# Optimization experiments

Measured on AMD Instinct MI355X. Metric: run time of the kernel, lower is better.

## Reference

```python
import jax, jax.numpy as jnp
import numpy as np

D = 3  # hardcoded window half-width in the module


def setup_inputs() -> dict:
    key = jax.random.key(0)
    ks = jax.random.split(key, 5)
    B, T, S = 16, 1024, 4096
    q_size, c_size, p_size = 512, 512, 512
    q = jax.random.normal(ks[0], (B, q_size, S), jnp.float32)
    c_t = jax.random.normal(ks[1], (B, T, c_size), jnp.float32)
    # torch nn.Linear weight layouts: (out_features, in_features)
    W_a = jax.random.normal(ks[2], (c_size, q_size), jnp.float32) / np.sqrt(q_size).astype(np.float32)
    W_p = jax.random.normal(ks[3], (p_size, c_size), jnp.float32) / np.sqrt(c_size).astype(np.float32)
    V_p = jax.random.normal(ks[4], (1, p_size), jnp.float32) / np.sqrt(p_size).astype(np.float32)
    return {"q": q, "c_t": c_t, "W_a": W_a, "W_p": W_p, "V_p": V_p}


def reference(q, c_t, W_a, W_p, V_p):
    B, q_size, S = q.shape
    # predictive alignment: p_t = S * sigmoid(V_p tanh(W_p c_t)) -> (B, T, 1)
    p_t = S * jax.nn.sigmoid(jnp.tanh(c_t @ W_p.T) @ V_p.T)
    # pad one NaN column at the front of the sequence, then (B, S+1, q_size)
    q_pad = jnp.pad(q, ((0, 0), (0, 0), (1, 0)), constant_values=jnp.nan).transpose(0, 2, 1)
    # window indices: clamp(long(p_t) + idx + 1, 0, S+1) % (S+1), idx in [-D, D]
    offsets = jnp.arange(-D + 1, D + 2)  # (2D+1,)
    s = jnp.clip(p_t.astype(jnp.int32) + offsets[None, None, :], 0, S + 1) % (S + 1)  # (B,T,2D+1)
    # per-batch gather of the local window: (B, T, 2D+1, q_size)
    qg = q_pad[jnp.arange(B)[:, None, None], s]
    nan_loc = jnp.isnan(qg[..., 0])  # (B, T, 2D+1)
    qg = jnp.where(nan_loc[..., None], 0.0, qg)
    # score: dot(W_a q, c_t) -> (B, T, 2D+1)
    a_t = jnp.einsum('btwq,cq,btc->btw', qg, W_a, c_t)
    a_t = jnp.where(nan_loc, -jnp.inf, a_t)
    attn = jax.nn.softmax(a_t, axis=2)
    # Gaussian decay around predicted position p_t
    gauss = jnp.exp(-2.0 * ((jnp.clip(s.astype(jnp.float32) - 1.0, 0.0, None) - p_t) / D) ** 2)
    W_attn = attn * gauss
    out = jnp.einsum('btw,btwq->btq', W_attn, qg)  # (B, T, q_size)
    return out
```

## Files before the change

kernel.cpp:

```cpp
#include <hip/hip_runtime.h>
#include <hip/hip_bf16.h>

#define BB 16
#define TT 1024
#define SS 4096
#define CS 512
#define QS 512
#define PS 512
#define NROW (BB*TT)

typedef unsigned short ushort_t;
typedef unsigned int u32;
typedef short bf16x8 __attribute__((ext_vector_type(8)));
typedef float f32x4 __attribute__((ext_vector_type(4)));

#define AS1 __attribute__((address_space(1)))
#define AS3 __attribute__((address_space(3)))

__device__ __forceinline__ void gl2l16(const void* g, void* l) {
    __builtin_amdgcn_global_load_lds((const AS1 u32*)g, (AS3 u32*)l, 16, 0, 0);
}

__device__ __forceinline__ ushort_t f2bf(float f) {
    u32 x = __float_as_uint(f);
    return (ushort_t)((x + 0x7fffu + ((x >> 16) & 1u)) >> 16);
}
__device__ __forceinline__ float bf2f(ushort_t b) {
    return __uint_as_float(((u32)b) << 16);
}

__global__ __launch_bounds__(256) void k_conv_a(const float* __restrict__ c,
                                                ushort_t* __restrict__ A) {
    const int i = blockIdx.x * 256 + threadIdx.x;
    const int m = i >> 7;
    const int k = (i & 127) * 4;
    float4 v = *(const float4*)(c + (size_t)m * CS + k);
    ushort4 hi, lo;
    hi.x = f2bf(v.x); lo.x = f2bf(v.x - bf2f(hi.x));
    hi.y = f2bf(v.y); lo.y = f2bf(v.y - bf2f(hi.y));
    hi.z = f2bf(v.z); lo.z = f2bf(v.z - bf2f(hi.z));
    hi.w = f2bf(v.w); lo.w = f2bf(v.w - bf2f(hi.w));
    *(ushort4*)(A + (size_t)m * 1024 + k)       = hi;
    *(ushort4*)(A + (size_t)m * 1024 + 512 + k) = lo;
}

__global__ __launch_bounds__(256) void k_conv_b(const float* __restrict__ Wa,
                                                const float* __restrict__ Wp,
                                                ushort_t* __restrict__ B,
                                                int* __restrict__ cnt) {
    const int n = blockIdx.x;
    const int t = threadIdx.x;
    if (n == 0 && t < 2) cnt[t] = 0;
    #pragma unroll
    for (int kk = 0; kk < 2; ++kk) {
        const int k = t + 256 * kk;
        float v = (n < 512) ? Wa[(size_t)k * QS + n] : Wp[(size_t)(n - 512) * CS + k];
        ushort_t hi = f2bf(v);
        ushort_t lo = f2bf(v - bf2f(hi));
        B[(size_t)n * 1024 + k]       = hi;
        B[(size_t)n * 1024 + 512 + k] = lo;
    }
}

__global__ __launch_bounds__(256) void k_tq(const float* __restrict__ q,
                                            float* __restrict__ qT) {
    __shared__ float t[64][65];
    const int b  = blockIdx.z;
    const int s0 = blockIdx.x * 64;
    const int d0 = blockIdx.y * 64;
    const int tx = threadIdx.x & 15;
    const int ty = threadIdx.x >> 4;
    const float* qb = q + ((size_t)b * QS + d0) * SS + s0;
    #pragma unroll
    for (int i = 0; i < 4; ++i) {
        float4 v = *(const float4*)(qb + (size_t)(ty + 16 * i) * SS + tx * 4);
        *(float4*)&t[ty + 16 * i][tx * 4] = v;
    }
    __syncthreads();
    float* qo = qT + ((size_t)b * SS + s0) * QS + d0;
    #pragma unroll
    for (int i = 0; i < 4; ++i) {
        const int s = ty + 16 * i;
        float4 v = make_float4(t[tx * 4 + 0][s], t[tx * 4 + 1][s],
                               t[tx * 4 + 2][s], t[tx * 4 + 3][s]);
        *(float4*)(qo + (size_t)s * QS + tx * 4) = v;
    }
}

__global__ __launch_bounds__(512, 2) void k_gemm(const ushort_t* __restrict__ A,
                                                 const ushort_t* __restrict__ B,
                                                 const float* __restrict__ V_p,
                                                 float* __restrict__ u,
                                                 float* __restrict__ zpart) {
    __shared__ ushort_t lds[8][8192];
    const int tid = threadIdx.x;
    const int l = tid & 63;
    const int w = tid >> 6;
    const int wm = w >> 2;
    const int wn = w & 3;
    const int ln = l & 15, lh = l >> 4;

    const int orig = blockIdx.x;
    const int swz = ((orig & 7) << 5) + (orig >> 3);
    const int m0 = (swz >> 2) * 256;
    const int nt = swz & 3;
    const int n0 = nt * 256;

    const int srow = tid >> 2;
    const int scg  = tid & 3;
    const int scol0 = (scg ^ ((srow >> 1) & 3)) * 8;

    const int swzr = (lh ^ ((ln >> 1) & 3)) << 3;
    int aoffL[2][4], boffL[4];
    #pragma unroll
    for (int ms = 0; ms < 2; ++ms)
        #pragma unroll
        for (int mi = 0; mi < 4; ++mi)
            aoffL[ms][mi] = (wm * 128 + ms * 64 + mi * 16 + ln) * 32 + swzr;
    #pragma unroll
    for (int ni = 0; ni < 4; ++ni)
        boffL[ni] = (wn * 64 + ni * 16 + ln) * 32 + swzr;

    f32x4 acc[8][4];
    #pragma unroll
    for (int a = 0; a < 8; ++a)
        #pragma unroll
        for (int b2 = 0; b2 < 4; ++b2) acc[a][b2] = (f32x4){0.f, 0.f, 0.f, 0.f};

    auto STAGE = [&](int c) {
        const int tt = c >> 2, rem = c & 3, kh = rem >> 1;
        const int blk = tt >> 3, k0 = (tt & 7) << 6;
        const ushort_t* src;
        if (rem & 1) {
            const int boff = (blk == 1) ? 512 : 0;
            src = B + (size_t)(n0 + srow) * 1024 + boff + k0 + kh * 32 + scol0;
        } else {
            const int aoff = (blk == 2) ? 512 : 0;
            src = A + (size_t)(m0 + srow) * 1024 + aoff + k0 + kh * 32 + scol0;
        }
        ushort_t* dst = &lds[c & 7][tid * 8];
        gl2l16(src, dst);
        gl2l16(src + 128 * 1024, dst + 4096);
    };

    #pragma unroll
    for (int c = 0; c < 6; ++c) STAGE(c);
    asm volatile("s_waitcnt vmcnt(4)" ::: "memory");
    __builtin_amdgcn_s_barrier();

    #pragma unroll 1
    for (int t = 0; t < 24; ++t) {
        #pragma unroll
        for (int P = 0; P < 2; ++P) {
            const int sA = ((t << 2) + (P << 1)) & 7;
            const int sB = sA + 1;
            const ushort_t* bA = &lds[sA][0];
            const ushort_t* bB = &lds[sB][0];
            bf16x8 af[8], bb[4];
            #pragma unroll
            for (int mi = 0; mi < 4; ++mi) {
                af[mi]     = *(const bf16x8*)(bA + aoffL[0][mi]);
                af[4 + mi] = *(const bf16x8*)(bA + aoffL[1][mi]);
            }
            #pragma unroll
            for (int ni = 0; ni < 4; ++ni)
                bb[ni] = *(const bf16x8*)(bB + boffL[ni]);
            const int c0 = (t << 2) + (P << 1) + 6;
            if (c0 <= 95) STAGE(c0);
            if (c0 + 1 <= 95) STAGE(c0 + 1);
            __builtin_amdgcn_s_setprio(1);
            #pragma unroll
            for (int ms = 0; ms < 2; ++ms)
                #pragma unroll
                for (int mi = 0; mi < 4; ++mi)
                    #pragma unroll
                    for (int ni = 0; ni < 4; ++ni)
                        acc[ms * 4 + mi][ni] = __builtin_amdgcn_mfma_f32_16x16x32_bf16(
                            af[ms * 4 + mi], bb[ni], acc[ms * 4 + mi][ni], 0, 0, 0);
            __builtin_amdgcn_s_setprio(0);
            if (P == 1) {
                if (t == 22) { asm volatile("s_waitcnt vmcnt(0)" ::: "memory"); }
                else if (t < 22) { asm volatile("s_waitcnt vmcnt(4)" ::: "memory"); }
            }
            __builtin_amdgcn_s_barrier();
        }
    }

    if (nt < 2) {
        #pragma unroll
        for (int mg = 0; mg < 8; ++mg) {
            #pragma unroll
            for (int r = 0; r < 4; ++r) {
                const int m = m0 + wm * 128 + mg * 16 + lh * 4 + r;
                float* up = u + (size_t)m * QS + nt * 256 + wn * 64 + ln;
                #pragma unroll
                for (int ni = 0; ni < 4; ++ni) up[ni * 16] = acc[mg][ni][r];
            }
        }
    } else {
        float vp[4];
        #pragma unroll
        for (int ni = 0; ni < 4; ++ni)
            vp[ni] = V_p[(nt - 2) * 256 + wn * 64 + ni * 16 + ln];
        #pragma unroll
        for (int mg = 0; mg < 8; ++mg) {
            #pragma unroll
            for (int r = 0; r < 4; ++r) {
                float sv = 0.f;
                #pragma unroll
                for (int ni = 0; ni < 4; ++ni) sv += tanhf(acc[mg][ni][r]) * vp[ni];
                sv += __shfl_xor(sv, 1, 64);
                sv += __shfl_xor(sv, 2, 64);
                sv += __shfl_xor(sv, 4, 64);
                sv += __shfl_xor(sv, 8, 64);
                if (ln == 0)
                    zpart[(size_t)(m0 + wm * 128 + mg * 16 + lh * 4 + r) * 8 +
                          (nt - 2) * 4 + wn] = sv;
            }
        }
    }
}

__global__ __launch_bounds__(256) void k_z(const float* __restrict__ zpart,
                                           float* __restrict__ pt, int* __restrict__ tr,
                                           int* __restrict__ list1, int* __restrict__ cnt1) {
    const int row = blockIdx.x * 256 + threadIdx.x;
    const float4 a = *(const float4*)(zpart + (size_t)row * 8);
    const float4 b = *(const float4*)(zpart + (size_t)row * 8 + 4);
    float z = ((a.x + a.y) + (a.z + a.w)) + ((b.x + b.y) + (b.z + b.w));
    float ptv = 4096.f / (1.f + expf(-z));
    float fr = ptv - floorf(ptv);
    pt[row] = ptv;
    tr[row] = (int)ptv;
    if (fr < 0.06f || fr > 0.94f) {
        int i = atomicAdd(cnt1, 1);
        list1[i] = row;
    }
}

__global__ __launch_bounds__(256) void k_rep1(
    const float* __restrict__ c_t, const float* __restrict__ W_p,
    const float* __restrict__ V_p, float* __restrict__ pt, int* __restrict__ tr,
    const int* __restrict__ list1, const int* __restrict__ cnt1,
    int* __restrict__ list2, int* __restrict__ cnt2)
{
    const int tid = threadIdx.x;
    const int lane = tid & 63;
    const int wid = tid >> 6;
    const int n1 = cnt1[0];
    __shared__ float cl[8][132 * 4];
    __shared__ double zl[4][8];
    __shared__ int rows_s[8];

    for (int g0 = blockIdx.x * 8; g0 < n1; g0 += gridDim.x * 8) {
        const int nr = min(8, n1 - g0);
        __syncthreads();
        if (tid < nr) rows_s[tid] = list1[g0 + tid];
        __syncthreads();
        for (int idx = tid; idx < nr * 128; idx += 256) {
            int r = idx >> 7, k = (idx & 127) * 4;
            *(float4*)&cl[r][k] = *(const float4*)(c_t + (size_t)rows_s[r] * CS + k);
        }
        __syncthreads();

        const float* wp0 = W_p + (size_t)tid * CS;
        const float* wp1 = W_p + (size_t)(tid + 256) * CS;
        f32x4 acc[2][8];
        #pragma unroll
        for (int p = 0; p < 2; ++p)
            #pragma unroll
            for (int r = 0; r < 8; ++r) acc[p][r] = (f32x4){0.f, 0.f, 0.f, 0.f};

        for (int k = 0; k < CS; k += 16) {
            f32x4 w0[4], w1[4];
            #pragma unroll
            for (int j = 0; j < 4; ++j) {
                w0[j] = *(const f32x4*)(wp0 + k + 4 * j);
                w1[j] = *(const f32x4*)(wp1 + k + 4 * j);
            }
            #pragma unroll
            for (int j = 0; j < 4; ++j) {
                #pragma unroll
                for (int r = 0; r < 8; ++r) {
                    f32x4 c4 = *(const f32x4*)&cl[r][k + 4 * j];
                    acc[0][r] += c4 * w0[j];
                    acc[1][r] += c4 * w1[j];
                }
            }
        }

        const float vp0 = V_p[tid];
        const float vp1 = V_p[tid + 256];
        double zp[8];
        #pragma unroll
        for (int r = 0; r < 8; ++r) {
            float X0 = (acc[0][r][0] + acc[0][r][1]) + (acc[0][r][2] + acc[0][r][3]);
            float X1 = (acc[1][r][0] + acc[1][r][1]) + (acc[1][r][2] + acc[1][r][3]);
            zp[r] = (double)(tanhf(X0) * vp0) + (double)(tanhf(X1) * vp1);
        }
        #pragma unroll
        for (int r = 0; r < 8; ++r) {
            double v = zp[r];
            #pragma unroll
            for (int o = 32; o > 0; o >>= 1) v += __shfl_down(v, o, 64);
            if (lane == 0) zl[wid][r] = v;
        }
        __syncthreads();
        if (tid < nr) {
            double z = (zl[0][tid] + zl[1][tid]) + (zl[2][tid] + zl[3][tid]);
            double ptv = 4096.0 / (1.0 + exp(-z));
            const int row = rows_s[tid];
            pt[row] = (float)ptv;
            tr[row] = (int)ptv;
            double fr = ptv - floor(ptv);
            if (fr < 5e-3 || fr > 0.995) {
                int i2 = atomicAdd(cnt2, 1);
                list2[i2] = row;
            }
        }
    }
}

__global__ __launch_bounds__(256) void k_rep2a(
    const float* __restrict__ c_t, const float* __restrict__ W_p,
    const float* __restrict__ V_p,
    const int* __restrict__ list2, const int* __restrict__ cnt2,
    double* __restrict__ zp2)
{
    const int tid = threadIdx.x;
    const int pl = tid & 63;
    const int kq = tid >> 6;
    const int n2 = cnt2[0];
    __shared__ float cl[CS];
    __shared__ double xsh[4][64];

    for (int i = blockIdx.x; i < n2 * 8; i += gridDim.x) {
        const int li = i >> 3;
        const int pc = i & 7;
        const int row = list2[li];
        const int p0 = pc * 64;
        __syncthreads();
        if (tid < 128)
            *(float4*)(cl + tid * 4) = *(const float4*)(c_t + (size_t)row * CS + tid * 4);
        __syncthreads();
        const float* wr = W_p + (size_t)(p0 + pl) * CS + kq * 128;
        const float* cr = cl + kq * 128;
        double Xa = 0.0, Xb = 0.0, Xc = 0.0, Xd = 0.0;
        #pragma unroll 4
        for (int k = 0; k < 128; k += 4) {
            float4 w4 = *(const float4*)(wr + k);
            float4 c4 = *(const float4*)(cr + k);
            Xa += (double)c4.x * w4.x;
            Xb += (double)c4.y * w4.y;
            Xc += (double)c4.z * w4.z;
            Xd += (double)c4.w * w4.w;
        }
        xsh[kq][pl] = (Xa + Xb) + (Xc + Xd);
        __syncthreads();
        if (tid < 64) {
            double X = (xsh[0][pl] + xsh[1][pl]) + (xsh[2][pl] + xsh[3][pl]);
            double zv = tanh(X) * (double)V_p[p0 + pl];
            #pragma unroll
            for (int o = 32; o > 0; o >>= 1) zv += __shfl_down(zv, o, 64);
            if (pl == 0) zp2[i] = zv;
        }
    }
}

__global__ __launch_bounds__(256) void k_rep2b(
    const double* __restrict__ zp2, const int* __restrict__ list2,
    const int* __restrict__ cnt2, float* __restrict__ pt, int* __restrict__ tr)
{
    const int idx = blockIdx.x * 256 + threadIdx.x;
    if (idx >= cnt2[0]) return;
    const double* zr = zp2 + (size_t)idx * 8;
    double z = 0.0;
    #pragma unroll
    for (int j = 0; j < 8; ++j) z += zr[j];
    double ptv = 4096.0 / (1.0 + exp(-z));
    const int row = list2[idx];
    pt[row] = (float)ptv;
    tr[row] = (int)ptv;
}

__global__ __launch_bounds__(256) void k_attn_t(
    const float* __restrict__ qT, const float* __restrict__ u,
    const float* __restrict__ pt, const int* __restrict__ tr,
    float* __restrict__ out)
{
    const int wid = threadIdx.x >> 6;
    const int lane = threadIdx.x & 63;
    const int bt = blockIdx.x * 4 + wid;
    const int b = bt >> 10;

    const float* urow = u + (size_t)bt * QS;
    float4 ua = *(const float4*)(urow + lane * 8);
    float4 ub = *(const float4*)(urow + lane * 8 + 4);
    float uv[8] = {ua.x, ua.y, ua.z, ua.w, ub.x, ub.y, ub.z, ub.w};

    const float ptv = pt[bt];
    const int tn = tr[bt];
    const float* qTb = qT + (size_t)b * SS * QS;

    bool val[7];
    int pos[7];
    #pragma unroll
    for (int w = 0; w < 7; ++w) {
        int sv = tn + w - 2;
        sv = sv < 0 ? 0 : (sv > SS + 1 ? SS + 1 : sv);
        if (sv == SS + 1) sv = 0;
        val[w] = (sv != 0);
        pos[w] = sv - 1;
    }

    float qg[7][8];
    #pragma unroll
    for (int w = 0; w < 7; ++w) {
        if (val[w]) {
            const float* qr = qTb + (size_t)pos[w] * QS + lane * 8;
            float4 a = *(const float4*)qr;
            float4 c = *(const float4*)(qr + 4);
            qg[w][0] = a.x; qg[w][1] = a.y; qg[w][2] = a.z; qg[w][3] = a.w;
            qg[w][4] = c.x; qg[w][5] = c.y; qg[w][6] = c.z; qg[w][7] = c.w;
        } else {
            #pragma unroll
            for (int j = 0; j < 8; ++j) qg[w][j] = 0.f;
        }
    }

    float at[7];
    #pragma unroll
    for (int w = 0; w < 7; ++w) {
        float p = 0.f;
        #pragma unroll
        for (int j = 0; j < 8; ++j) p = fmaf(qg[w][j], uv[j], p);
        #pragma unroll
        for (int o = 1; o < 64; o <<= 1) p += __shfl_xor(p, o, 64);
        at[w] = p;
    }

    float m = -1e30f;
    #pragma unroll
    for (int w = 0; w < 7; ++w) if (val[w]) m = fmaxf(m, at[w]);
    float e[7], den = 0.f;
    #pragma unroll
    for (int w = 0; w < 7; ++w) { e[w] = val[w] ? expf(at[w] - m) : 0.f; den += e[w]; }
    const float inv = 1.f / den;

    float acc[8] = {0.f, 0.f, 0.f, 0.f, 0.f, 0.f, 0.f, 0.f};
    #pragma unroll
    for (int w = 0; w < 7; ++w) {
        if (val[w]) {
            float d = ((float)pos[w] - ptv) * (1.f / 3.f);
            float wt = e[w] * inv * expf(-2.f * d * d);
            #pragma unroll
            for (int j = 0; j < 8; ++j) acc[j] = fmaf(wt, qg[w][j], acc[j]);
        }
    }

    float* orow = out + (size_t)bt * QS + lane * 8;
    *(float4*)orow       = make_float4(acc[0], acc[1], acc[2], acc[3]);
    *(float4*)(orow + 4) = make_float4(acc[4], acc[5], acc[6], acc[7]);
}

__global__ __launch_bounds__(256) void k_attn_g(
    const float* __restrict__ q, const float* __restrict__ u,
    const float* __restrict__ pt, const int* __restrict__ tr,
    float* __restrict__ out)
{
    const int wid = threadIdx.x >> 6;
    const int lane = threadIdx.x & 63;
    const int bt = blockIdx.x * 4 + wid;
    const int b = bt >> 10;

    const float* urow = u + (size_t)bt * QS;
    float4 ua = *(const float4*)(urow + lane * 8);
    float4 ub = *(const float4*)(urow + lane * 8 + 4);
    float uv[8] = {ua.x, ua.y, ua.z, ua.w, ub.x, ub.y, ub.z, ub.w};

    const float ptv = pt[bt];
    const int tn = tr[bt];
    const float* qb = q + (size_t)b * QS * SS;

    bool val[7];
    int pos[7];
    #pragma unroll
    for (int w = 0; w < 7; ++w) {
        int sv = tn + w - 2;
        sv = sv < 0 ? 0 : (sv > SS + 1 ? SS + 1 : sv);
        if (sv == SS + 1) sv = 0;
        val[w] = (sv != 0);
        pos[w] = sv - 1;
    }

    float qg[7][8];
    #pragma unroll
    for (int j = 0; j < 8; ++j) {
        const float* qrow = qb + (size_t)(lane * 8 + j) * SS;
        #pragma unroll
        for (int w = 0; w < 7; ++w)
            qg[w][j] = val[w] ? qrow[pos[w]] : 0.f;
    }

    float at[7];
    #pragma unroll
    for (int w = 0; w < 7; ++w) {
        float p = 0.f;
        #pragma unroll
        for (int j = 0; j < 8; ++j) p = fmaf(qg[w][j], uv[j], p);
        #pragma unroll
        for (int o = 1; o < 64; o <<= 1) p += __shfl_xor(p, o, 64);
        at[w] = p;
    }

    float m = -1e30f;
    #pragma unroll
    for (int w = 0; w < 7; ++w) if (val[w]) m = fmaxf(m, at[w]);
    float e[7], den = 0.f;
    #pragma unroll
    for (int w = 0; w < 7; ++w) { e[w] = val[w] ? expf(at[w] - m) : 0.f; den += e[w]; }
    const float inv = 1.f / den;

    float acc[8] = {0.f, 0.f, 0.f, 0.f, 0.f, 0.f, 0.f, 0.f};
    #pragma unroll
    for (int w = 0; w < 7; ++w) {
        if (val[w]) {
            float d = ((float)pos[w] - ptv) * (1.f / 3.f);
            float wt = e[w] * inv * expf(-2.f * d * d);
            #pragma unroll
            for (int j = 0; j < 8; ++j) acc[j] = fmaf(wt, qg[w][j], acc[j]);
        }
    }

    float* orow = out + (size_t)bt * QS + lane * 8;
    *(float4*)orow       = make_float4(acc[0], acc[1], acc[2], acc[3]);
    *(float4*)(orow + 4) = make_float4(acc[4], acc[5], acc[6], acc[7]);
}

extern "C" void kernel_launch(void* const* d_in, const int* in_sizes, int n_in,
                              void* d_out, int out_size, void* d_ws, size_t ws_size,
                              hipStream_t stream) {
    const float* q   = (const float*)d_in[0];
    const float* c_t = (const float*)d_in[1];
    const float* W_a = (const float*)d_in[2];
    const float* W_p = (const float*)d_in[3];
    const float* V_p = (const float*)d_in[4];
    float* out = (float*)d_out;

    char* ws = (char*)d_ws;
    ushort_t* Ap  = (ushort_t*)(ws);
    ushort_t* Bp  = (ushort_t*)(ws + 33554432);
    float*    u   = (float*)  (ws + 35651584);
    float*    zp  = (float*)  (ws + 69206016);
    float*    pt  = (float*)  (ws + 69730304);
    int*      tr  = (int*)    (ws + 69795840);
    int*      l1  = (int*)    (ws + 69861376);
    int*      l2  = (int*)    (ws + 69926912);
    int*      cnt = (int*)    (ws + 69992448);
    double*   zp2 = (double*) (ws + 70000640);
    float*    qT  = (float*)  (ws + 73400320);
    const bool use_T = (ws_size >= 73400320ULL + 134217728ULL);

    hipLaunchKernelGGL(k_conv_a, dim3(8192), dim3(256), 0, stream, c_t, Ap);
    hipLaunchKernelGGL(k_conv_b, dim3(1024), dim3(256), 0, stream, W_a, W_p, Bp, cnt);
    if (use_T)
        hipLaunchKernelGGL(k_tq, dim3(64, 8, 16), dim3(256), 0, stream, q, qT);
    hipLaunchKernelGGL(k_gemm, dim3(256), dim3(512), 0, stream, Ap, Bp, V_p, u, zp);
    hipLaunchKernelGGL(k_z, dim3(64), dim3(256), 0, stream, zp, pt, tr, l1, cnt);
    hipLaunchKernelGGL(k_rep1, dim3(512), dim3(256), 0, stream,
                       c_t, W_p, V_p, pt, tr, l1, cnt, l2, cnt + 1);
    hipLaunchKernelGGL(k_rep2a, dim3(512), dim3(256), 0, stream,
                       c_t, W_p, V_p, l2, cnt + 1, zp2);
    hipLaunchKernelGGL(k_rep2b, dim3(64), dim3(256), 0, stream,
                       zp2, l2, cnt + 1, pt, tr);
    if (use_T)
        hipLaunchKernelGGL(k_attn_t, dim3(NROW / 4), dim3(256), 0, stream, qT, u, pt, tr, out);
    else
        hipLaunchKernelGGL(k_attn_g, dim3(NROW / 4), dim3(256), 0, stream, q, u, pt, tr, out);
}
```

Baseline: 249.3 us.

## Load GEMM B fragments from global, rewrite transpose without LDS, reorder launches

The GEMM main loop now streams only the A operand through LDS with global_load_lds. B fragments are loaded straight from global memory into registers and double-buffered across half-steps, with explicit waitcnt and sched barriers placed around the MFMA blocks. This is meant to halve LDS staging traffic and raise MFMA density, at the cost of more global loads and VGPR pressure under the 512x2 launch bound. The q transpose kernel drops its LDS tile in favour of a per-thread 4x4 register transpose, and it now launches just before the attention kernel instead of before the GEMM.

```diff
diff --git a/kernel.cpp b/kernel.cpp
--- a/kernel.cpp
+++ b/kernel.cpp
@@ -64,27 +64,19 @@
 
 __global__ __launch_bounds__(256) void k_tq(const float* __restrict__ q,
                                             float* __restrict__ qT) {
-    __shared__ float t[64][65];
     const int b  = blockIdx.z;
-    const int s0 = blockIdx.x * 64;
-    const int d0 = blockIdx.y * 64;
-    const int tx = threadIdx.x & 15;
-    const int ty = threadIdx.x >> 4;
+    const int s0 = blockIdx.x * 64 + (threadIdx.x & 15) * 4;
+    const int d0 = blockIdx.y * 64 + (threadIdx.x >> 4) * 4;
     const float* qb = q + ((size_t)b * QS + d0) * SS + s0;
-    #pragma unroll
-    for (int i = 0; i < 4; ++i) {
-        float4 v = *(const float4*)(qb + (size_t)(ty + 16 * i) * SS + tx * 4);
-        *(float4*)&t[ty + 16 * i][tx * 4] = v;
-    }
-    __syncthreads();
+    float4 v0 = *(const float4*)(qb);
+    float4 v1 = *(const float4*)(qb + SS);
+    float4 v2 = *(const float4*)(qb + 2 * SS);
+    float4 v3 = *(const float4*)(qb + 3 * SS);
     float* qo = qT + ((size_t)b * SS + s0) * QS + d0;
-    #pragma unroll
-    for (int i = 0; i < 4; ++i) {
-        const int s = ty + 16 * i;
-        float4 v = make_float4(t[tx * 4 + 0][s], t[tx * 4 + 1][s],
-                               t[tx * 4 + 2][s], t[tx * 4 + 3][s]);
-        *(float4*)(qo + (size_t)s * QS + tx * 4) = v;
-    }
+    *(float4*)(qo)          = make_float4(v0.x, v1.x, v2.x, v3.x);
+    *(float4*)(qo + QS)     = make_float4(v0.y, v1.y, v2.y, v3.y);
+    *(float4*)(qo + 2 * QS) = make_float4(v0.z, v1.z, v2.z, v3.z);
+    *(float4*)(qo + 3 * QS) = make_float4(v0.w, v1.w, v2.w, v3.w);
 }
 
 __global__ __launch_bounds__(512, 2) void k_gemm(const ushort_t* __restrict__ A,
@@ -111,15 +103,14 @@
     const int scol0 = (scg ^ ((srow >> 1) & 3)) * 8;
 
     const int swzr = (lh ^ ((ln >> 1) & 3)) << 3;
-    int aoffL[2][4], boffL[4];
+    int aoffL[2][4];
     #pragma unroll
     for (int ms = 0; ms < 2; ++ms)
         #pragma unroll
         for (int mi = 0; mi < 4; ++mi)
             aoffL[ms][mi] = (wm * 128 + ms * 64 + mi * 16 + ln) * 32 + swzr;
-    #pragma unroll
-    for (int ni = 0; ni < 4; ++ni)
-        boffL[ni] = (wn * 64 + ni * 16 + ln) * 32 + swzr;
+
+    const ushort_t* bbase = B + (size_t)(n0 + wn * 64 + ln) * 1024 + lh * 8;
 
     f32x4 acc[8][4];
     #pragma unroll
@@ -127,63 +118,67 @@
         #pragma unroll
         for (int b2 = 0; b2 < 4; ++b2) acc[a][b2] = (f32x4){0.f, 0.f, 0.f, 0.f};
 
-    auto STAGE = [&](int c) {
-        const int tt = c >> 2, rem = c & 3, kh = rem >> 1;
-        const int blk = tt >> 3, k0 = (tt & 7) << 6;
-        const ushort_t* src;
-        if (rem & 1) {
-            const int boff = (blk == 1) ? 512 : 0;
-            src = B + (size_t)(n0 + srow) * 1024 + boff + k0 + kh * 32 + scol0;
-        } else {
-            const int aoff = (blk == 2) ? 512 : 0;
-            src = A + (size_t)(m0 + srow) * 1024 + aoff + k0 + kh * 32 + scol0;
-        }
+    bf16x8 af[8], bb0[4], bb1[4];
+
+    auto STAGEA = [&](int c) {
+        const int tt2 = c >> 1, kh2 = c & 1;
+        const int blk2 = tt2 >> 3, k02 = (tt2 & 7) << 6;
+        const int aoff2 = (blk2 == 2) ? 512 : 0;
+        const ushort_t* src = A + (size_t)(m0 + srow) * 1024 + aoff2 + k02 +
+                              kh2 * 32 + scol0;
         ushort_t* dst = &lds[c & 7][tid * 8];
         gl2l16(src, dst);
         gl2l16(src + 128 * 1024, dst + 4096);
     };
-
-    #pragma unroll
-    for (int c = 0; c < 6; ++c) STAGE(c);
+    auto LOADB = [&](bf16x8* bbv, int g) {
+        const int tt2 = g >> 1, kh2 = g & 1;
+        const int blk2 = tt2 >> 3;
+        const int off2 = ((blk2 == 1) ? 512 : 0) + ((tt2 & 7) << 6) + kh2 * 32;
+        #pragma unroll
+        for (int ni = 0; ni < 4; ++ni)
+            bbv[ni] = *(const bf16x8*)(bbase + (size_t)ni * 16 * 1024 + off2);
+    };
+    auto LDA = [&](int slot) {
+        const ushort_t* bA = &lds[slot][0];
+        #pragma unroll
+        for (int ms = 0; ms < 2; ++ms)
+            #pragma unroll
+            for (int mi = 0; mi < 4; ++mi)
+                af[ms * 4 + mi] = *(const bf16x8*)(bA + aoffL[ms][mi]);
+    };
+    auto MFMAC = [&](const bf16x8* bbv) {
+        asm volatile("s_waitcnt vmcnt(6)" ::: "memory");
+        asm volatile("s_waitcnt lgkmcnt(0)" ::: "memory");
+        __builtin_amdgcn_sched_barrier(0);
+        __builtin_amdgcn_s_setprio(1);
+        #pragma unroll
+        for (int ms = 0; ms < 2; ++ms)
+            #pragma unroll
+            for (int mi = 0; mi < 4; ++mi)
+                #pragma unroll
+                for (int ni = 0; ni < 4; ++ni)
+                    acc[ms * 4 + mi][ni] = __builtin_amdgcn_mfma_f32_16x16x32_bf16(
+                        af[ms * 4 + mi], bbv[ni], acc[ms * 4 + mi][ni], 0, 0, 0);
+        __builtin_amdgcn_s_setprio(0);
+        __builtin_amdgcn_s_barrier();
+    };
+
+    #pragma unroll
+    for (int c = 0; c < 6; ++c) STAGEA(c);
+    LOADB(bb0, 0);
     asm volatile("s_waitcnt vmcnt(4)" ::: "memory");
     __builtin_amdgcn_s_barrier();
 
     #pragma unroll 1
     for (int t = 0; t < 24; ++t) {
-        #pragma unroll
-        for (int P = 0; P < 2; ++P) {
-            const int sA = ((t << 2) + (P << 1)) & 7;
-            const int sB = sA + 1;
-            const ushort_t* bA = &lds[sA][0];
-            const ushort_t* bB = &lds[sB][0];
-            bf16x8 af[8], bb[4];
-            #pragma unroll
-            for (int mi = 0; mi < 4; ++mi) {
-                af[mi]     = *(const bf16x8*)(bA + aoffL[0][mi]);
-                af[4 + mi] = *(const bf16x8*)(bA + aoffL[1][mi]);
-            }
-            #pragma unroll
-            for (int ni = 0; ni < 4; ++ni)
-                bb[ni] = *(const bf16x8*)(bB + boffL[ni]);
-            const int c0 = (t << 2) + (P << 1) + 6;
-            if (c0 <= 95) STAGE(c0);
-            if (c0 + 1 <= 95) STAGE(c0 + 1);
-            __builtin_amdgcn_s_setprio(1);
-            #pragma unroll
-            for (int ms = 0; ms < 2; ++ms)
-                #pragma unroll
-                for (int mi = 0; mi < 4; ++mi)
-                    #pragma unroll
-                    for (int ni = 0; ni < 4; ++ni)
-                        acc[ms * 4 + mi][ni] = __builtin_amdgcn_mfma_f32_16x16x32_bf16(
-                            af[ms * 4 + mi], bb[ni], acc[ms * 4 + mi][ni], 0, 0, 0);
-            __builtin_amdgcn_s_setprio(0);
-            if (P == 1) {
-                if (t == 22) { asm volatile("s_waitcnt vmcnt(0)" ::: "memory"); }
-                else if (t < 22) { asm volatile("s_waitcnt vmcnt(4)" ::: "memory"); }
-            }
-            __builtin_amdgcn_s_barrier();
-        }
+        LDA((2 * t) & 7);
+        LOADB(bb1, 2 * t + 1);
+        if (2 * t + 6 <= 47) STAGEA(2 * t + 6);
+        MFMAC(bb0);
+        LDA((2 * t + 1) & 7);
+        if (t < 23) LOADB(bb0, 2 * t + 2);
+        if (2 * t + 7 <= 47) STAGEA(2 * t + 7);
+        MFMAC(bb1);
     }
 
     if (nt < 2) {
@@ -563,8 +558,6 @@
 
     hipLaunchKernelGGL(k_conv_a, dim3(8192), dim3(256), 0, stream, c_t, Ap);
     hipLaunchKernelGGL(k_conv_b, dim3(1024), dim3(256), 0, stream, W_a, W_p, Bp, cnt);
-    if (use_T)
-        hipLaunchKernelGGL(k_tq, dim3(64, 8, 16), dim3(256), 0, stream, q, qT);
     hipLaunchKernelGGL(k_gemm, dim3(256), dim3(512), 0, stream, Ap, Bp, V_p, u, zp);
     hipLaunchKernelGGL(k_z, dim3(64), dim3(256), 0, stream, zp, pt, tr, l1, cnt);
     hipLaunchKernelGGL(k_rep1, dim3(512), dim3(256), 0, stream,
@@ -573,8 +566,10 @@
                        c_t, W_p, V_p, l2, cnt + 1, zp2);
     hipLaunchKernelGGL(k_rep2b, dim3(64), dim3(256), 0, stream,
                        zp2, l2, cnt + 1, pt, tr);
-    if (use_T)
+    if (use_T) {
+        hipLaunchKernelGGL(k_tq, dim3(64, 8, 16), dim3(256), 0, stream, q, qT);
         hipLaunchKernelGGL(k_attn_t, dim3(NROW / 4), dim3(256), 0, stream, qT, u, pt, tr, out);
-    else
+    } else {
         hipLaunchKernelGGL(k_attn_g, dim3(NROW / 4), dim3(256), 0, stream, q, u, pt, tr, out);
-}
+    }
+}
```

New measurement: 270.1 us. 8.3% more time.

## Use 1024-thread GEMM blocks, register-only q transpose, and reorder transpose launch

Applied to the files above, without the earlier changes.

The GEMM block grows from 8 to 16 waves, each wave owning a 64x64 tile instead of 128x64. Each thread now stages one 16-byte chunk instead of two, and the vmcnt waits are adjusted to match. The q transpose drops its LDS tile and swaps 4x4 float4 blocks in registers, which makes each store row a strided 16-byte write. The transpose launch moves to just before the attention kernel, presumably so its output is fresher in cache when consumed. Risks are occupancy limits at 1024 threads with launch_bounds(1024,4), and poorer coalescing in the transpose stores.

```diff
diff --git a/kernel.cpp b/kernel.cpp
--- a/kernel.cpp
+++ b/kernel.cpp
@@ -64,34 +64,26 @@
 
 __global__ __launch_bounds__(256) void k_tq(const float* __restrict__ q,
                                             float* __restrict__ qT) {
-    __shared__ float t[64][65];
     const int b  = blockIdx.z;
-    const int s0 = blockIdx.x * 64;
-    const int d0 = blockIdx.y * 64;
-    const int tx = threadIdx.x & 15;
-    const int ty = threadIdx.x >> 4;
+    const int s0 = blockIdx.x * 64 + (threadIdx.x & 15) * 4;
+    const int d0 = blockIdx.y * 64 + (threadIdx.x >> 4) * 4;
     const float* qb = q + ((size_t)b * QS + d0) * SS + s0;
-    #pragma unroll
-    for (int i = 0; i < 4; ++i) {
-        float4 v = *(const float4*)(qb + (size_t)(ty + 16 * i) * SS + tx * 4);
-        *(float4*)&t[ty + 16 * i][tx * 4] = v;
-    }
-    __syncthreads();
+    float4 v0 = *(const float4*)(qb);
+    float4 v1 = *(const float4*)(qb + SS);
+    float4 v2 = *(const float4*)(qb + 2 * SS);
+    float4 v3 = *(const float4*)(qb + 3 * SS);
     float* qo = qT + ((size_t)b * SS + s0) * QS + d0;
-    #pragma unroll
-    for (int i = 0; i < 4; ++i) {
-        const int s = ty + 16 * i;
-        float4 v = make_float4(t[tx * 4 + 0][s], t[tx * 4 + 1][s],
-                               t[tx * 4 + 2][s], t[tx * 4 + 3][s]);
-        *(float4*)(qo + (size_t)s * QS + tx * 4) = v;
-    }
-}
-
-__global__ __launch_bounds__(512, 2) void k_gemm(const ushort_t* __restrict__ A,
-                                                 const ushort_t* __restrict__ B,
-                                                 const float* __restrict__ V_p,
-                                                 float* __restrict__ u,
-                                                 float* __restrict__ zpart) {
+    *(float4*)(qo)          = make_float4(v0.x, v1.x, v2.x, v3.x);
+    *(float4*)(qo + QS)     = make_float4(v0.y, v1.y, v2.y, v3.y);
+    *(float4*)(qo + 2 * QS) = make_float4(v0.z, v1.z, v2.z, v3.z);
+    *(float4*)(qo + 3 * QS) = make_float4(v0.w, v1.w, v2.w, v3.w);
+}
+
+__global__ __launch_bounds__(1024, 4) void k_gemm(const ushort_t* __restrict__ A,
+                                                  const ushort_t* __restrict__ B,
+                                                  const float* __restrict__ V_p,
+                                                  float* __restrict__ u,
+                                                  float* __restrict__ zpart) {
     __shared__ ushort_t lds[8][8192];
     const int tid = threadIdx.x;
     const int l = tid & 63;
@@ -111,19 +103,17 @@
     const int scol0 = (scg ^ ((srow >> 1) & 3)) * 8;
 
     const int swzr = (lh ^ ((ln >> 1) & 3)) << 3;
-    int aoffL[2][4], boffL[4];
-    #pragma unroll
-    for (int ms = 0; ms < 2; ++ms)
-        #pragma unroll
-        for (int mi = 0; mi < 4; ++mi)
-            aoffL[ms][mi] = (wm * 128 + ms * 64 + mi * 16 + ln) * 32 + swzr;
+    int aoffL[4], boffL[4];
+    #pragma unroll
+    for (int mi = 0; mi < 4; ++mi)
+        aoffL[mi] = (wm * 64 + mi * 16 + ln) * 32 + swzr;
     #pragma unroll
     for (int ni = 0; ni < 4; ++ni)
         boffL[ni] = (wn * 64 + ni * 16 + ln) * 32 + swzr;
 
-    f32x4 acc[8][4];
-    #pragma unroll
-    for (int a = 0; a < 8; ++a)
+    f32x4 acc[4][4];
+    #pragma unroll
+    for (int a = 0; a < 4; ++a)
         #pragma unroll
         for (int b2 = 0; b2 < 4; ++b2) acc[a][b2] = (f32x4){0.f, 0.f, 0.f, 0.f};
 
@@ -138,14 +128,12 @@
             const int aoff = (blk == 2) ? 512 : 0;
             src = A + (size_t)(m0 + srow) * 1024 + aoff + k0 + kh * 32 + scol0;
         }
-        ushort_t* dst = &lds[c & 7][tid * 8];
-        gl2l16(src, dst);
-        gl2l16(src + 128 * 1024, dst + 4096);
+        gl2l16(src, &lds[c & 7][tid * 8]);
     };
 
     #pragma unroll
     for (int c = 0; c < 6; ++c) STAGE(c);
-    asm volatile("s_waitcnt vmcnt(4)" ::: "memory");
+    asm volatile("s_waitcnt vmcnt(2)" ::: "memory");
     __builtin_amdgcn_s_barrier();
 
     #pragma unroll 1
@@ -156,12 +144,10 @@
             const int sB = sA + 1;
             const ushort_t* bA = &lds[sA][0];
             const ushort_t* bB = &lds[sB][0];
-            bf16x8 af[8], bb[4];
-            #pragma unroll
-            for (int mi = 0; mi < 4; ++mi) {
-                af[mi]     = *(const bf16x8*)(bA + aoffL[0][mi]);
-                af[4 + mi] = *(const bf16x8*)(bA + aoffL[1][mi]);
-            }
+            bf16x8 af[4], bb[4];
+            #pragma unroll
+            for (int mi = 0; mi < 4; ++mi)
+                af[mi] = *(const bf16x8*)(bA + aoffL[mi]);
             #pragma unroll
             for (int ni = 0; ni < 4; ++ni)
                 bb[ni] = *(const bf16x8*)(bB + boffL[ni]);
@@ -170,17 +156,15 @@
             if (c0 + 1 <= 95) STAGE(c0 + 1);
             __builtin_amdgcn_s_setprio(1);
             #pragma unroll
-            for (int ms = 0; ms < 2; ++ms)
+            for (int mi = 0; mi < 4; ++mi)
                 #pragma unroll
-                for (int mi = 0; mi < 4; ++mi)
-                    #pragma unroll
-                    for (int ni = 0; ni < 4; ++ni)
-                        acc[ms * 4 + mi][ni] = __builtin_amdgcn_mfma_f32_16x16x32_bf16(
-                            af[ms * 4 + mi], bb[ni], acc[ms * 4 + mi][ni], 0, 0, 0);
+                for (int ni = 0; ni < 4; ++ni)
+                    acc[mi][ni] = __builtin_amdgcn_mfma_f32_16x16x32_bf16(
+                        af[mi], bb[ni], acc[mi][ni], 0, 0, 0);
             __builtin_amdgcn_s_setprio(0);
             if (P == 1) {
                 if (t == 22) { asm volatile("s_waitcnt vmcnt(0)" ::: "memory"); }
-                else if (t < 22) { asm volatile("s_waitcnt vmcnt(4)" ::: "memory"); }
+                else if (t < 22) { asm volatile("s_waitcnt vmcnt(2)" ::: "memory"); }
             }
             __builtin_amdgcn_s_barrier();
         }
@@ -188,13 +172,13 @@
 
     if (nt < 2) {
         #pragma unroll
-        for (int mg = 0; mg < 8; ++mg) {
+        for (int mi = 0; mi < 4; ++mi) {
             #pragma unroll
             for (int r = 0; r < 4; ++r) {
-                const int m = m0 + wm * 128 + mg * 16 + lh * 4 + r;
+                const int m = m0 + wm * 64 + mi * 16 + lh * 4 + r;
                 float* up = u + (size_t)m * QS + nt * 256 + wn * 64 + ln;
                 #pragma unroll
-                for (int ni = 0; ni < 4; ++ni) up[ni * 16] = acc[mg][ni][r];
+                for (int ni = 0; ni < 4; ++ni) up[ni * 16] = acc[mi][ni][r];
             }
         }
     } else {
@@ -203,18 +187,18 @@
         for (int ni = 0; ni < 4; ++ni)
             vp[ni] = V_p[(nt - 2) * 256 + wn * 64 + ni * 16 + ln];
         #pragma unroll
-        for (int mg = 0; mg < 8; ++mg) {
+        for (int mi = 0; mi < 4; ++mi) {
             #pragma unroll
             for (int r = 0; r < 4; ++r) {
                 float sv = 0.f;
                 #pragma unroll
-                for (int ni = 0; ni < 4; ++ni) sv += tanhf(acc[mg][ni][r]) * vp[ni];
+                for (int ni = 0; ni < 4; ++ni) sv += tanhf(acc[mi][ni][r]) * vp[ni];
                 sv += __shfl_xor(sv, 1, 64);
                 sv += __shfl_xor(sv, 2, 64);
                 sv += __shfl_xor(sv, 4, 64);
                 sv += __shfl_xor(sv, 8, 64);
                 if (ln == 0)
-                    zpart[(size_t)(m0 + wm * 128 + mg * 16 + lh * 4 + r) * 8 +
+                    zpart[(size_t)(m0 + wm * 64 + mi * 16 + lh * 4 + r) * 8 +
                           (nt - 2) * 4 + wn] = sv;
             }
         }
@@ -563,9 +547,7 @@
 
     hipLaunchKernelGGL(k_conv_a, dim3(8192), dim3(256), 0, stream, c_t, Ap);
     hipLaunchKernelGGL(k_conv_b, dim3(1024), dim3(256), 0, stream, W_a, W_p, Bp, cnt);
-    if (use_T)
-        hipLaunchKernelGGL(k_tq, dim3(64, 8, 16), dim3(256), 0, stream, q, qT);
-    hipLaunchKernelGGL(k_gemm, dim3(256), dim3(512), 0, stream, Ap, Bp, V_p, u, zp);
+    hipLaunchKernelGGL(k_gemm, dim3(256), dim3(1024), 0, stream, Ap, Bp, V_p, u, zp);
     hipLaunchKernelGGL(k_z, dim3(64), dim3(256), 0, stream, zp, pt, tr, l1, cnt);
     hipLaunchKernelGGL(k_rep1, dim3(512), dim3(256), 0, stream,
                        c_t, W_p, V_p, pt, tr, l1, cnt, l2, cnt + 1);
@@ -573,8 +555,10 @@
                        c_t, W_p, V_p, l2, cnt + 1, zp2);
     hipLaunchKernelGGL(k_rep2b, dim3(64), dim3(256), 0, stream,
                        zp2, l2, cnt + 1, pt, tr);
-    if (use_T)
+    if (use_T) {
+        hipLaunchKernelGGL(k_tq, dim3(64, 8, 16), dim3(256), 0, stream, q, qT);
         hipLaunchKernelGGL(k_attn_t, dim3(NROW / 4), dim3(256), 0, stream, qT, u, pt, tr, out);
-    else
+    } else {
         hipLaunchKernelGGL(k_attn_g, dim3(NROW / 4), dim3(256), 0, stream, q, u, pt, tr, out);
-}
+    }
+}
```

Measured after the change: 240.9 us. -3.4%, faster.
